# Kernel tuning notes

Hardware: AMD Instinct MI355X
Metric: run time of the kernel (lower is better)

## Reference

```python
import jax, jax.numpy as jnp
import numpy as np

D_MODEL = 2048
SSM_RANK = 4            # ultimate_config.ar_ssm_max_rank
FFN_RANK = max(D_MODEL // 128, 2)  # = 16
EPS = 1e-6


def rmsnorm(x, w):
    # shared RMSNorm: x * w / rms(x)
    ms = jnp.mean(jnp.square(x), axis=-1, keepdims=True)
    return x * jax.lax.rsqrt(ms + EPS) * w


def ar_ssm(x, V, U, a_logit):
    # low-rank (rank r) semiseparable SSM:
    #   u_t = V^T x_t            [B,S,r]
    #   h_t = a * h_{t-1} + u_t  (per-rank learned decay a in (0,1))
    #   y_t = U h_t              [B,S,D]
    a = jax.nn.sigmoid(a_logit)               # [r]
    u = jnp.einsum('bsd,dr->bsr', x, V)       # [B,S,r]
    u_t = jnp.swapaxes(u, 0, 1)               # [S,B,r]

    def step(h, u_s):
        h = a * h + u_s
        return h, h

    h0 = jnp.zeros(u_t.shape[1:], dtype=x.dtype)   # [B,r]
    h_last, hs = jax.lax.scan(step, h0, u_t)        # hs: [S,B,r]
    hs = jnp.swapaxes(hs, 0, 1)                     # [B,S,r]
    y = jnp.einsum('bsr,dr->bsd', hs, U)
    return y, h_last


def ffn(x, W1, W2):
    return jnp.einsum('bsr,rd->bsd', jax.nn.gelu(jnp.einsum('bsd,dr->bsr', x, W1)), W2)


def setup_inputs() -> dict:
    key = jax.random.key(0)
    ks = jax.random.split(key, 7)
    B, S, D, R, RF = 4, 4096, D_MODEL, SSM_RANK, FFN_RANK
    x = jax.random.normal(ks[0], (B, S, D), dtype=jnp.float32)
    norm_w = jnp.ones((D,), dtype=jnp.float32)
    V = jax.random.normal(ks[1], (D, R), dtype=jnp.float32) / np.sqrt(D)
    U = jax.random.normal(ks[2], (D, R), dtype=jnp.float32) / np.sqrt(R)
    a_logit = jax.random.normal(ks[3], (R,), dtype=jnp.float32)
    W1 = jax.random.normal(ks[4], (D, RF), dtype=jnp.float32) / np.sqrt(D)
    W2 = jax.random.normal(ks[5], (RF, D), dtype=jnp.float32) / np.sqrt(RF)
    return {"x": x, "norm_w": norm_w, "V": V, "U": U, "a_logit": a_logit, "W1": W1, "W2": W2}


def reference(x, norm_w, V, U, a_logit, W1, W2):
    x_ar, _ = ar_ssm(rmsnorm(x, norm_w), V, U, a_logit)
    x = x + x_ar
    x = x + ffn(rmsnorm(x, norm_w), W1, W2)
    return x
```

## Files before the change

### kernel.cpp

```cpp
#include <hip/hip_runtime.h>
#include <math.h>
#include <stdint.h>

#define D 2048
#define S_LEN 4096
#define NB 4
#define NTOK (NB * S_LEN)

__device__ __forceinline__ float gelu_tanh(float v) {
    const float c = 0.7978845608028654f;
    float t = tanhf(c * (v + 0.044715f * v * v * v));
    return 0.5f * v * (1.0f + t);
}

__device__ __forceinline__ void gload_lds16(const float* g, float* l) {
    __builtin_amdgcn_global_load_lds(
        (const __attribute__((address_space(1))) void*)g,
        (__attribute__((address_space(3))) void*)(uintptr_t)(uint32_t)(uintptr_t)l,
        16, 0, 0);
}

__global__ __launch_bounds__(256) void k0_transpose(
        const float* __restrict__ W1, const float* __restrict__ V, const float* __restrict__ U,
        float* __restrict__ W1t, float* __restrict__ Vt, float* __restrict__ Ut)
{
    const int id = blockIdx.x * 256 + threadIdx.x;
    if (id < D * 16) {
        const int d = id >> 4, f = id & 15;
        W1t[f * D + d] = W1[id];
    } else if (id < D * 16 + D * 4) {
        const int i2 = id - D * 16;
        Vt[(i2 & 3) * D + (i2 >> 2)] = V[i2];
    } else {
        const int i2 = id - D * 16 - D * 4;
        Ut[(i2 & 3) * D + (i2 >> 2)] = U[i2];
    }
}

__global__ __launch_bounds__(256) void k1_u_kernel(
        const float* __restrict__ x, const float* __restrict__ nw,
        const float* __restrict__ Vt, float* __restrict__ u)
{
    __shared__ float lw[10240];
    const int w = threadIdx.x >> 6;
    const int lane  = threadIdx.x & 63;
    const int t0 = ((blockIdx.x * 256 + threadIdx.x) >> 6) * 2;

    for (int s = w; s < 40; s += 4) {
        const int base = s * 256;
        const float* src = (base < 2048) ? (nw + base) : (Vt + base - 2048);
        gload_lds16(src + lane * 4, &lw[base + lane * 4]);
    }
    __syncthreads();

    float ss[2] = {0.f, 0.f};
    float uv[2][4] = {};

    #pragma unroll
    for (int j = 0; j < 8; ++j) {
        const int d0 = j * 256 + lane * 4;
        const float4 nw4 = *reinterpret_cast<const float4*>(lw + d0);
        float4 z4[2];
        #pragma unroll
        for (int tk = 0; tk < 2; ++tk) {
            const float4 xv = *reinterpret_cast<const float4*>(x + (size_t)(t0 + tk) * D + d0);
            ss[tk] += xv.x*xv.x + xv.y*xv.y + xv.z*xv.z + xv.w*xv.w;
            z4[tk].x = xv.x*nw4.x; z4[tk].y = xv.y*nw4.y;
            z4[tk].z = xv.z*nw4.z; z4[tk].w = xv.w*nw4.w;
        }
        #pragma unroll
        for (int r = 0; r < 4; ++r) {
            const float4 vv = *reinterpret_cast<const float4*>(lw + 2048 + r * 2048 + d0);
            #pragma unroll
            for (int tk = 0; tk < 2; ++tk)
                uv[tk][r] += z4[tk].x*vv.x + z4[tk].y*vv.y + z4[tk].z*vv.z + z4[tk].w*vv.w;
        }
    }
    #pragma unroll
    for (int m = 1; m < 64; m <<= 1) {
        #pragma unroll
        for (int tk = 0; tk < 2; ++tk) {
            ss[tk] += __shfl_xor(ss[tk], m);
            #pragma unroll
            for (int r = 0; r < 4; ++r) uv[tk][r] += __shfl_xor(uv[tk][r], m);
        }
    }
    if (lane < 8) {
        float ssv = ss[0], uvv = uv[0][0];
        #pragma unroll
        for (int tk = 0; tk < 2; ++tk)
            #pragma unroll
            for (int r = 0; r < 4; ++r)
                if (lane == tk * 4 + r) { ssv = ss[tk]; uvv = uv[tk][r]; }
        const float rstd = rsqrtf(ssv * (1.0f / 2048.0f) + 1e-6f);
        u[(size_t)t0 * 4 + lane] = rstd * uvv;
    }
}

__global__ __launch_bounds__(1024) void k2_scan_kernel(
        const float* __restrict__ u, const float* __restrict__ a_logit,
        float* __restrict__ hs)
{
    __shared__ float4 lds[1024];
    const int b = blockIdx.x;
    const int i = threadIdx.x;
    const float4 al4 = *reinterpret_cast<const float4*>(a_logit);
    float4 a;
    a.x = 1.0f / (1.0f + expf(-al4.x));
    a.y = 1.0f / (1.0f + expf(-al4.y));
    a.z = 1.0f / (1.0f + expf(-al4.z));
    a.w = 1.0f / (1.0f + expf(-al4.w));
    const float4* up = reinterpret_cast<const float4*>(u) + (size_t)b * S_LEN;
    float4*       hp = reinterpret_cast<float4*>(hs)      + (size_t)b * S_LEN;

    const int s0 = i * 4;
    float4 ul[4];
    float4 h; h.x = 0.f; h.y = 0.f; h.z = 0.f; h.w = 0.f;
    #pragma unroll
    for (int k = 0; k < 4; ++k) {
        ul[k] = up[s0 + k];
        h.x = a.x * h.x + ul[k].x; h.y = a.y * h.y + ul[k].y;
        h.z = a.z * h.z + ul[k].z; h.w = a.w * h.w + ul[k].w;
    }

    float4 m;
    m.x = a.x*a.x; m.y = a.y*a.y; m.z = a.z*a.z; m.w = a.w*a.w;
    m.x *= m.x; m.y *= m.y; m.z *= m.z; m.w *= m.w;
    float4 run = h;
    lds[i] = run;
    for (int off = 1; off < 1024; off <<= 1) {
        __syncthreads();
        float4 v;
        if (i >= off) v = lds[i - off];
        else { v.x = 0.f; v.y = 0.f; v.z = 0.f; v.w = 0.f; }
        __syncthreads();
        run.x += m.x * v.x; run.y += m.y * v.y;
        run.z += m.z * v.z; run.w += m.w * v.w;
        lds[i] = run;
        m.x *= m.x; m.y *= m.y; m.z *= m.z; m.w *= m.w;
    }
    __syncthreads();
    float4 hh;
    if (i == 0) { hh.x = 0.f; hh.y = 0.f; hh.z = 0.f; hh.w = 0.f; }
    else hh = lds[i - 1];
    #pragma unroll
    for (int k = 0; k < 4; ++k) {
        hh.x = a.x * hh.x + ul[k].x; hh.y = a.y * hh.y + ul[k].y;
        hh.z = a.z * hh.z + ul[k].z; hh.w = a.w * hh.w + ul[k].w;
        hp[s0 + k] = hh;
    }
}

#define SLICE_F 5376
__global__ __launch_bounds__(256) void k3_fused_kernel(
        const float* __restrict__ x, const float* __restrict__ nw,
        const float* __restrict__ Ut, const float* __restrict__ hs,
        const float* __restrict__ W1t, const float* __restrict__ W2,
        float* __restrict__ out)
{
    __shared__ float buf[2][SLICE_F];
    __shared__ float reds[4][2][20];
    __shared__ float tvs[4][32];
    const int w = threadIdx.x >> 6;
    const int lane = threadIdx.x & 63;
    const int t0 = (blockIdx.x * 4 + w) * 2;
    const float4* hs4 = reinterpret_cast<const float4*>(hs);
    float4 hv[2];
    #pragma unroll
    for (int tk = 0; tk < 2; ++tk) hv[tk] = hs4[t0 + tk];

    float ss[2] = {0.f, 0.f};
    float pf[2][16] = {};

    for (int s = w; s < 21; s += 4) {
        const float* src = (s == 0) ? (nw)
                         : (s < 5)  ? (Ut + (size_t)(s - 1) * D)
                                    : (W1t + (size_t)(s - 5) * D);
        gload_lds16(src + lane * 4, &buf[0][s * 256 + lane * 4]);
    }
    __syncthreads();

    for (int j = 0; j < 8; ++j) {
        const int cur = j & 1;
        if (j < 7) {
            const int jn = (j + 1) * 256;
            for (int s = w; s < 21; s += 4) {
                const float* src = (s == 0) ? (nw + jn)
                                 : (s < 5)  ? (Ut + (size_t)(s - 1) * D + jn)
                                            : (W1t + (size_t)(s - 5) * D + jn);
                gload_lds16(src + lane * 4, &buf[cur ^ 1][s * 256 + lane * 4]);
            }
        }
        const float* bw = buf[cur];
        const int d0 = j * 256 + lane * 4;
        const float4 nw4 = *reinterpret_cast<const float4*>(bw + lane * 4);
        float4 ut[4];
        #pragma unroll
        for (int r = 0; r < 4; ++r)
            ut[r] = *reinterpret_cast<const float4*>(bw + 256 + r * 256 + lane * 4);
        float4 z4[2];
        #pragma unroll
        for (int tk = 0; tk < 2; ++tk) {
            const float4 xv = *reinterpret_cast<const float4*>(x + (size_t)(t0 + tk) * D + d0);
            const float x20 = xv.x + hv[tk].x*ut[0].x + hv[tk].y*ut[1].x + hv[tk].z*ut[2].x + hv[tk].w*ut[3].x;
            const float x21 = xv.y + hv[tk].x*ut[0].y + hv[tk].y*ut[1].y + hv[tk].z*ut[2].y + hv[tk].w*ut[3].y;
            const float x22 = xv.z + hv[tk].x*ut[0].z + hv[tk].y*ut[1].z + hv[tk].z*ut[2].z + hv[tk].w*ut[3].z;
            const float x23 = xv.w + hv[tk].x*ut[0].w + hv[tk].y*ut[1].w + hv[tk].z*ut[2].w + hv[tk].w*ut[3].w;
            ss[tk] += x20*x20 + x21*x21 + x22*x22 + x23*x23;
            z4[tk].x = x20*nw4.x; z4[tk].y = x21*nw4.y;
            z4[tk].z = x22*nw4.z; z4[tk].w = x23*nw4.w;
        }
        #pragma unroll
        for (int f = 0; f < 16; ++f) {
            const float4 wv = *reinterpret_cast<const float4*>(bw + 1280 + f * 256 + lane * 4);
            #pragma unroll
            for (int tk = 0; tk < 2; ++tk)
                pf[tk][f] += z4[tk].x*wv.x + z4[tk].y*wv.y + z4[tk].z*wv.z + z4[tk].w*wv.w;
        }
        __syncthreads();
    }

    #pragma unroll
    for (int m = 1; m < 64; m <<= 1) {
        #pragma unroll
        for (int tk = 0; tk < 2; ++tk) {
            ss[tk] += __shfl_xor(ss[tk], m);
            #pragma unroll
            for (int f = 0; f < 16; ++f) pf[tk][f] += __shfl_xor(pf[tk][f], m);
        }
    }
    if (lane == 0) {
        #pragma unroll
        for (int tk = 0; tk < 2; ++tk) {
            reds[w][tk][16] = ss[tk];
            #pragma unroll
            for (int f = 0; f < 16; ++f) reds[w][tk][f] = pf[tk][f];
        }
    }
    __syncthreads();
    if (lane < 32) {
        const int mytk = lane >> 4, myf = lane & 15;
        const float rstd = rsqrtf(reds[w][mytk][16] * (1.0f / 2048.0f) + 1e-6f);
        tvs[w][lane] = gelu_tanh(rstd * reds[w][mytk][myf]);
    }
    __syncthreads();
    float tvv[2][16];
    #pragma unroll
    for (int tk = 0; tk < 2; ++tk)
        #pragma unroll
        for (int f = 0; f < 16; ++f) tvv[tk][f] = tvs[w][tk * 16 + f];

    for (int s = w; s < 20; s += 4) {
        const float* src = (s < 4) ? (Ut + (size_t)s * D)
                                   : (W2 + (size_t)(s - 4) * D);
        gload_lds16(src + lane * 4, &buf[0][s * 256 + lane * 4]);
    }
    __syncthreads();

    for (int j = 0; j < 8; ++j) {
        const int cur = j & 1;
        if (j < 7) {
            const int jn = (j + 1) * 256;
            for (int s = w; s < 20; s += 4) {
                const float* src = (s < 4) ? (Ut + (size_t)s * D + jn)
                                           : (W2 + (size_t)(s - 4) * D + jn);
                gload_lds16(src + lane * 4, &buf[cur ^ 1][s * 256 + lane * 4]);
            }
        }
        const float* bw = buf[cur];
        const int d0 = j * 256 + lane * 4;
        float4 ut[4];
        #pragma unroll
        for (int r = 0; r < 4; ++r)
            ut[r] = *reinterpret_cast<const float4*>(bw + r * 256 + lane * 4);
        float4 acc[2];
        #pragma unroll
        for (int tk = 0; tk < 2; ++tk) {
            const float4 xv = *reinterpret_cast<const float4*>(x + (size_t)(t0 + tk) * D + d0);
            acc[tk].x = xv.x + hv[tk].x*ut[0].x + hv[tk].y*ut[1].x + hv[tk].z*ut[2].x + hv[tk].w*ut[3].x;
            acc[tk].y = xv.y + hv[tk].x*ut[0].y + hv[tk].y*ut[1].y + hv[tk].z*ut[2].y + hv[tk].w*ut[3].y;
            acc[tk].z = xv.z + hv[tk].x*ut[0].z + hv[tk].y*ut[1].z + hv[tk].z*ut[2].z + hv[tk].w*ut[3].z;
            acc[tk].w = xv.w + hv[tk].x*ut[0].w + hv[tk].y*ut[1].w + hv[tk].z*ut[2].w + hv[tk].w*ut[3].w;
        }
        #pragma unroll
        for (int f = 0; f < 16; ++f) {
            const float4 w2v = *reinterpret_cast<const float4*>(bw + 1024 + f * 256 + lane * 4);
            #pragma unroll
            for (int tk = 0; tk < 2; ++tk) {
                acc[tk].x += tvv[tk][f] * w2v.x;
                acc[tk].y += tvv[tk][f] * w2v.y;
                acc[tk].z += tvv[tk][f] * w2v.z;
                acc[tk].w += tvv[tk][f] * w2v.w;
            }
        }
        #pragma unroll
        for (int tk = 0; tk < 2; ++tk)
            *reinterpret_cast<float4*>(out + (size_t)(t0 + tk) * D + d0) = acc[tk];
        __syncthreads();
    }
}

extern "C" void kernel_launch(void* const* d_in, const int* in_sizes, int n_in,
                              void* d_out, int out_size, void* d_ws, size_t ws_size,
                              hipStream_t stream)
{
    (void)in_sizes; (void)n_in; (void)out_size; (void)ws_size;
    const float* x  = (const float*)d_in[0];
    const float* nw = (const float*)d_in[1];
    const float* V  = (const float*)d_in[2];
    const float* U  = (const float*)d_in[3];
    const float* al = (const float*)d_in[4];
    const float* W1 = (const float*)d_in[5];
    const float* W2 = (const float*)d_in[6];
    float* out = (float*)d_out;
    float* u   = (float*)d_ws;
    float* hs  = u + (size_t)NTOK * 4;
    float* W1t = hs + (size_t)NTOK * 4;
    float* Vt  = W1t + (size_t)16 * D;
    float* Ut  = Vt + (size_t)4 * D;

    k0_transpose  <<<dim3(192),       dim3(256),  0, stream>>>(W1, V, U, W1t, Vt, Ut);
    k1_u_kernel   <<<dim3(NTOK / 8),  dim3(256),  0, stream>>>(x, nw, Vt, u);
    k2_scan_kernel<<<dim3(NB),        dim3(1024), 0, stream>>>(u, al, hs);
    k3_fused_kernel<<<dim3(NTOK / 8), dim3(256),  0, stream>>>(x, nw, Ut, hs, W1t, W2, out);
}
```

Before: 320.7 us.

## Keep residual stream in registers in fused kernel; double tokens per wave in u kernel

The fused kernel now holds the post-SSM residual values (x + U h) in registers across both passes, so the second pass no longer re-reads x from global memory or recomputes the U-projection. It also drops Ut from the second-pass LDS staging. Separately, the u-projection kernel processes four tokens per wave instead of two, halving its grid and amortizing the LDS weight loads. The cost is higher register pressure (16 float4 per thread kept live plus fully unrolled loops), which could reduce occupancy or cause spills.

```diff
diff --git a/kernel.cpp b/kernel.cpp
--- a/kernel.cpp
+++ b/kernel.cpp
@@ -44,7 +44,7 @@
     __shared__ float lw[10240];
     const int w = threadIdx.x >> 6;
     const int lane  = threadIdx.x & 63;
-    const int t0 = ((blockIdx.x * 256 + threadIdx.x) >> 6) * 2;
+    const int t0 = (blockIdx.x * 4 + w) * 4;
 
     for (int s = w; s < 40; s += 4) {
         const int base = s * 256;
@@ -53,16 +53,16 @@
     }
     __syncthreads();
 
-    float ss[2] = {0.f, 0.f};
-    float uv[2][4] = {};
+    float ss[4] = {0.f, 0.f, 0.f, 0.f};
+    float uv[4][4] = {};
 
     #pragma unroll
     for (int j = 0; j < 8; ++j) {
         const int d0 = j * 256 + lane * 4;
         const float4 nw4 = *reinterpret_cast<const float4*>(lw + d0);
-        float4 z4[2];
-        #pragma unroll
-        for (int tk = 0; tk < 2; ++tk) {
+        float4 z4[4];
+        #pragma unroll
+        for (int tk = 0; tk < 4; ++tk) {
             const float4 xv = *reinterpret_cast<const float4*>(x + (size_t)(t0 + tk) * D + d0);
             ss[tk] += xv.x*xv.x + xv.y*xv.y + xv.z*xv.z + xv.w*xv.w;
             z4[tk].x = xv.x*nw4.x; z4[tk].y = xv.y*nw4.y;
@@ -72,23 +72,23 @@
         for (int r = 0; r < 4; ++r) {
             const float4 vv = *reinterpret_cast<const float4*>(lw + 2048 + r * 2048 + d0);
             #pragma unroll
-            for (int tk = 0; tk < 2; ++tk)
+            for (int tk = 0; tk < 4; ++tk)
                 uv[tk][r] += z4[tk].x*vv.x + z4[tk].y*vv.y + z4[tk].z*vv.z + z4[tk].w*vv.w;
         }
     }
     #pragma unroll
     for (int m = 1; m < 64; m <<= 1) {
         #pragma unroll
-        for (int tk = 0; tk < 2; ++tk) {
+        for (int tk = 0; tk < 4; ++tk) {
             ss[tk] += __shfl_xor(ss[tk], m);
             #pragma unroll
             for (int r = 0; r < 4; ++r) uv[tk][r] += __shfl_xor(uv[tk][r], m);
         }
     }
-    if (lane < 8) {
+    if (lane < 16) {
         float ssv = ss[0], uvv = uv[0][0];
         #pragma unroll
-        for (int tk = 0; tk < 2; ++tk)
+        for (int tk = 0; tk < 4; ++tk)
             #pragma unroll
             for (int r = 0; r < 4; ++r)
                 if (lane == tk * 4 + r) { ssv = ss[tk]; uvv = uv[tk][r]; }
@@ -171,6 +171,7 @@
 
     float ss[2] = {0.f, 0.f};
     float pf[2][16] = {};
+    float4 x2r[2][8];
 
     for (int s = w; s < 21; s += 4) {
         const float* src = (s == 0) ? (nw)
@@ -180,6 +181,7 @@
     }
     __syncthreads();
 
+    #pragma unroll
     for (int j = 0; j < 8; ++j) {
         const int cur = j & 1;
         if (j < 7) {
@@ -207,6 +209,8 @@
             const float x22 = xv.z + hv[tk].x*ut[0].z + hv[tk].y*ut[1].z + hv[tk].z*ut[2].z + hv[tk].w*ut[3].z;
             const float x23 = xv.w + hv[tk].x*ut[0].w + hv[tk].y*ut[1].w + hv[tk].z*ut[2].w + hv[tk].w*ut[3].w;
             ss[tk] += x20*x20 + x21*x21 + x22*x22 + x23*x23;
+            x2r[tk][j].x = x20; x2r[tk][j].y = x21;
+            x2r[tk][j].z = x22; x2r[tk][j].w = x23;
             z4[tk].x = x20*nw4.x; z4[tk].y = x21*nw4.y;
             z4[tk].z = x22*nw4.z; z4[tk].w = x23*nw4.w;
         }
@@ -250,41 +254,26 @@
         #pragma unroll
         for (int f = 0; f < 16; ++f) tvv[tk][f] = tvs[w][tk * 16 + f];
 
-    for (int s = w; s < 20; s += 4) {
-        const float* src = (s < 4) ? (Ut + (size_t)s * D)
-                                   : (W2 + (size_t)(s - 4) * D);
-        gload_lds16(src + lane * 4, &buf[0][s * 256 + lane * 4]);
-    }
-    __syncthreads();
-
+    for (int s = w; s < 16; s += 4)
+        gload_lds16(W2 + (size_t)s * D + lane * 4, &buf[0][s * 256 + lane * 4]);
+    __syncthreads();
+
+    #pragma unroll
     for (int j = 0; j < 8; ++j) {
         const int cur = j & 1;
         if (j < 7) {
             const int jn = (j + 1) * 256;
-            for (int s = w; s < 20; s += 4) {
-                const float* src = (s < 4) ? (Ut + (size_t)s * D + jn)
-                                           : (W2 + (size_t)(s - 4) * D + jn);
-                gload_lds16(src + lane * 4, &buf[cur ^ 1][s * 256 + lane * 4]);
-            }
+            for (int s = w; s < 16; s += 4)
+                gload_lds16(W2 + (size_t)s * D + jn + lane * 4, &buf[cur ^ 1][s * 256 + lane * 4]);
         }
         const float* bw = buf[cur];
         const int d0 = j * 256 + lane * 4;
-        float4 ut[4];
-        #pragma unroll
-        for (int r = 0; r < 4; ++r)
-            ut[r] = *reinterpret_cast<const float4*>(bw + r * 256 + lane * 4);
         float4 acc[2];
         #pragma unroll
-        for (int tk = 0; tk < 2; ++tk) {
-            const float4 xv = *reinterpret_cast<const float4*>(x + (size_t)(t0 + tk) * D + d0);
-            acc[tk].x = xv.x + hv[tk].x*ut[0].x + hv[tk].y*ut[1].x + hv[tk].z*ut[2].x + hv[tk].w*ut[3].x;
-            acc[tk].y = xv.y + hv[tk].x*ut[0].y + hv[tk].y*ut[1].y + hv[tk].z*ut[2].y + hv[tk].w*ut[3].y;
-            acc[tk].z = xv.z + hv[tk].x*ut[0].z + hv[tk].y*ut[1].z + hv[tk].z*ut[2].z + hv[tk].w*ut[3].z;
-            acc[tk].w = xv.w + hv[tk].x*ut[0].w + hv[tk].y*ut[1].w + hv[tk].z*ut[2].w + hv[tk].w*ut[3].w;
-        }
+        for (int tk = 0; tk < 2; ++tk) acc[tk] = x2r[tk][j];
         #pragma unroll
         for (int f = 0; f < 16; ++f) {
-            const float4 w2v = *reinterpret_cast<const float4*>(bw + 1024 + f * 256 + lane * 4);
+            const float4 w2v = *reinterpret_cast<const float4*>(bw + f * 256 + lane * 4);
             #pragma unroll
             for (int tk = 0; tk < 2; ++tk) {
                 acc[tk].x += tvv[tk][f] * w2v.x;
@@ -320,7 +309,7 @@
     float* Ut  = Vt + (size_t)4 * D;
 
     k0_transpose  <<<dim3(192),       dim3(256),  0, stream>>>(W1, V, U, W1t, Vt, Ut);
-    k1_u_kernel   <<<dim3(NTOK / 8),  dim3(256),  0, stream>>>(x, nw, Vt, u);
+    k1_u_kernel   <<<dim3(NTOK / 16), dim3(256),  0, stream>>>(x, nw, Vt, u);
     k2_scan_kernel<<<dim3(NB),        dim3(1024), 0, stream>>>(u, al, hs);
     k3_fused_kernel<<<dim3(NTOK / 8), dim3(256),  0, stream>>>(x, nw, Ut, hs, W1t, W2, out);
 }
```

Result: slower. 450.6 us (+40.5%).
